# Kernel tuning notes

Measured on AMD Instinct MI355X. Metric: run time of the kernel, lower is better.

Reference implementation:

```python
import jax, jax.numpy as jnp
import numpy as np
from jax import lax

EPS = 1e-5

def _bn_train(x, gamma, beta):
    # BatchNorm2d in training mode: batch stats over (N,H,W), biased variance
    mean = jnp.mean(x, axis=(0, 2, 3), keepdims=True)
    var = jnp.mean((x - mean) ** 2, axis=(0, 2, 3), keepdims=True)
    xhat = (x - mean) * lax.rsqrt(var + EPS)
    return gamma[None, :, None, None] * xhat + beta[None, :, None, None]

def _binact(x):
    # forward: sign(x); backward (STE): identity where |x|<=1, zero elsewhere
    y = jnp.where(jnp.abs(x) > 1.0, lax.stop_gradient(x), x)
    return y + lax.stop_gradient(jnp.sign(y) - y)

def _binconv(x, w, padding):
    # per-output-channel alpha = mean(|w|) over (in,kh,kw); w_bin = sign(w)*alpha with STE
    alpha = jnp.mean(jnp.abs(w), axis=(1, 2, 3), keepdims=True)
    w_bin = lax.stop_gradient(jnp.sign(w) * alpha - w) + w
    return lax.conv_general_dilated(
        x, w_bin, window_strides=(1, 1),
        padding=[(padding, padding), (padding, padding)],
        dimension_numbers=("NCHW", "OIHW", "NCHW"))

def setup_inputs() -> dict:
    key = jax.random.key(0)
    ks = jax.random.split(key, 10)
    B, Cin, Cout, H, W, T = 32, 128, 256, 64, 64, 512
    x = jax.random.normal(ks[0], (B, Cin, H, W), jnp.float32)
    t = jax.random.normal(ks[1], (B, T), jnp.float32)
    # conv weights, kaiming-ish scale
    w1 = jax.random.normal(ks[2], (Cout, Cin, 3, 3), jnp.float32) * (1.0 / np.sqrt(Cin * 9))
    w2 = jax.random.normal(ks[3], (Cout, Cout, 3, 3), jnp.float32) * (1.0 / np.sqrt(Cout * 9))
    wskip = jax.random.normal(ks[4], (Cout, Cin, 1, 1), jnp.float32) * (1.0 / np.sqrt(Cin))
    gamma1 = 1.0 + 0.1 * jax.random.normal(ks[5], (Cin,), jnp.float32)
    beta1 = 0.1 * jax.random.normal(ks[6], (Cin,), jnp.float32)
    gamma2 = 1.0 + 0.1 * jax.random.normal(ks[7], (Cout,), jnp.float32)
    beta2 = 0.1 * jax.random.normal(ks[8], (Cout,), jnp.float32)
    tw = jax.random.normal(ks[9], (Cout, T), jnp.float32) * (1.0 / np.sqrt(T))
    tb = jnp.zeros((Cout,), jnp.float32)
    return {"x": x, "t": t, "w1": w1, "w2": w2, "wskip": wskip,
            "gamma1": gamma1, "beta1": beta1, "gamma2": gamma2, "beta2": beta2,
            "tw": tw, "tb": tb}

def reference(x, t, w1, w2, wskip, gamma1, beta1, gamma2, beta2, tw, tb):
    h = _binconv(_binact(_bn_train(x, gamma1, beta1)), w1, padding=1)
    temb = t @ tw.T + tb                      # [B, Cout]
    h = h + temb[:, :, None, None]
    h = _binconv(_binact(_bn_train(h, gamma2, beta2)), w2, padding=1)
    return h + _binconv(x, wskip, padding=0)
```

## Files before the change

### kernel.cpp

```cpp
#include <hip/hip_runtime.h>
#include <stdint.h>

typedef unsigned short u16;
typedef uint8_t u8;
typedef __attribute__((ext_vector_type(8))) short short8;
typedef __attribute__((ext_vector_type(4))) float f32x4;
typedef __attribute__((ext_vector_type(4))) int i32x4;

#define EPSF 1e-5f
#define LGKM0 asm volatile("s_waitcnt lgkmcnt(0)" ::: "memory")
#define VM0   asm volatile("s_waitcnt vmcnt(0)" ::: "memory")
#define VM4   asm volatile("s_waitcnt vmcnt(4)" ::: "memory")
#define BAR   __builtin_amdgcn_s_barrier()
#define GLL(src, dst) __builtin_amdgcn_global_load_lds(                     \
    (const __attribute__((address_space(1))) void*)(src),                   \
    (__attribute__((address_space(3))) void*)(dst), 16, 0, 0)

__device__ __forceinline__ u16 f2bf(float f) {
  uint32_t u = __float_as_uint(f);
  u += 0x7FFFu + ((u >> 16) & 1u);
  return (u16)(u >> 16);
}
__device__ __forceinline__ u8 sgn8(float y) {
  return y > 0.f ? (u8)1 : (y < 0.f ? (u8)0xFF : (u8)0);
}

__global__ void bn1_stage1(const float* __restrict__ x, float* __restrict__ p1) {
  int c = blockIdx.x >> 2, s = blockIdx.x & 3;
  int tid = threadIdx.x;
  float sum = 0.f, sq = 0.f;
  for (int n = s * 8; n < s * 8 + 8; ++n) {
    const f32x4* bp = (const f32x4*)(x + (((size_t)(n * 128 + c)) << 12));
    #pragma unroll 4
    for (int i = tid; i < 1024; i += 256) {
      f32x4 v = bp[i];
      sum += v[0] + v[1] + v[2] + v[3];
      sq  += v[0]*v[0] + v[1]*v[1] + v[2]*v[2] + v[3]*v[3];
    }
  }
  __shared__ float rs[256], rq[256];
  rs[tid] = sum; rq[tid] = sq; __syncthreads();
  for (int st = 128; st > 0; st >>= 1) {
    if (tid < st) { rs[tid] += rs[tid + st]; rq[tid] += rq[tid + st]; }
    __syncthreads();
  }
  if (tid == 0) { p1[blockIdx.x] = rs[0]; p1[512 + blockIdx.x] = rq[0]; }
}

__global__ void bn1_stage2(const float* __restrict__ p1, const float* __restrict__ g,
                           const float* __restrict__ b, float* __restrict__ sc,
                           float* __restrict__ off) {
  int c = threadIdx.x;
  float s = 0.f, q = 0.f;
  for (int k = 0; k < 4; ++k) { s += p1[c * 4 + k]; q += p1[512 + c * 4 + k]; }
  float mean = s * (1.f / 131072.f);
  float var  = q * (1.f / 131072.f) - mean * mean;
  float is = rsqrtf(var + EPSF);
  float scv = g[c] * is;
  sc[c] = scv;
  off[c] = b[c] - mean * scv;
}

__global__ void bn2_stage2b(const float* __restrict__ pS, const float* __restrict__ pQ,
                            const float* __restrict__ g, const float* __restrict__ bb,
                            float* __restrict__ sc, float* __restrict__ off) {
  int o = blockIdx.x, t = threadIdx.x;
  __shared__ float rs[256], rq[256];
  float s = 0.f, q = 0.f;
  #pragma unroll
  for (int k = 0; k < 8; ++k) {
    size_t j = t + k * 256;
    s += pS[j * 256 + o];
    q += pQ[j * 256 + o];
  }
  rs[t] = s; rq[t] = q; __syncthreads();
  for (int st = 128; st > 0; st >>= 1) {
    if (t < st) { rs[t] += rs[t + st]; rq[t] += rq[t + st]; }
    __syncthreads();
  }
  if (t == 0) {
    float mean = rs[0] * (1.f / 131072.f);
    float var  = rq[0] * (1.f / 131072.f) - mean * mean;
    float is = rsqrtf(var + EPSF);
    float scv = g[o] * is;
    sc[o] = scv;
    off[o] = bb[o] - mean * scv;
  }
}

__device__ __forceinline__ float blk_reduce(float v, float* red) {
  int t = threadIdx.x;
  red[t] = v; __syncthreads();
  for (int st = 128; st > 0; st >>= 1) {
    if (t < st) red[t] += red[t + st];
    __syncthreads();
  }
  float r = red[0]; __syncthreads();
  return r;
}

__global__ void prep_weights(const float* __restrict__ w1, const float* __restrict__ w2,
                             const float* __restrict__ wsk, u8* __restrict__ w1s,
                             u8* __restrict__ w2s, u16* __restrict__ wskB,
                             float* __restrict__ alpha1, float* __restrict__ alpha2) {
  int o = blockIdx.x, t = threadIdx.x;
  int rg = o >> 6, ol = o & 63;
  __shared__ float red[256];
  float s = 0.f;
  for (int j = t; j < 1152; j += 256) s += fabsf(w1[(size_t)o * 1152 + j]);
  float a1 = blk_reduce(s, red) * (1.f / 1152.f);
  if (t == 0) alpha1[o] = a1;
  for (int j = t; j < 1152; j += 256) {
    int st = j >> 6, k = j & 63;
    int cc = st / 9, tap = st % 9;
    int ch = cc * 64 + k;
    int g = (ol << 2) + ((k >> 4) ^ ((ol >> 1) & 3));
    w1s[(size_t)st * 16384 + rg * 4096 + g * 16 + (k & 15)] =
        sgn8(w1[(size_t)o * 1152 + ch * 9 + tap]);
  }
  s = 0.f;
  for (int j = t; j < 2304; j += 256) s += fabsf(w2[(size_t)o * 2304 + j]);
  float a2 = blk_reduce(s, red) * (1.f / 2304.f);
  if (t == 0) alpha2[o] = a2;
  for (int j = t; j < 2304; j += 256) {
    int st = j >> 6, k = j & 63;
    int c4 = st / 9, tap = st % 9;
    int ch = c4 * 64 + k;
    int g = (ol << 2) + ((k >> 4) ^ ((ol >> 1) & 3));
    w2s[(size_t)st * 16384 + rg * 4096 + g * 16 + (k & 15)] =
        sgn8(w2[(size_t)o * 2304 + ch * 9 + tap]);
  }
  s = 0.f;
  for (int j = t; j < 128; j += 256) s += fabsf(wsk[o * 128 + j]);
  float ask = blk_reduce(s, red) * (1.f / 128.f);
  float ratio = ask / a2;
  for (int j = t; j < 128; j += 256) {
    int e = j >> 6, k = j & 63;
    float w = wsk[o * 128 + j];
    float v = w > 0.f ? ratio : (w < 0.f ? -ratio : 0.f);
    wskB[(size_t)e * 16384 + o * 64 + k] = f2bf(v);
  }
}

__global__ void temb_k(const float* __restrict__ t, const float* __restrict__ tw,
                       const float* __restrict__ tb, float* __restrict__ temb) {
  int bb = blockIdx.x, o = threadIdx.x;
  __shared__ float tl[512];
  tl[o] = t[bb * 512 + o];
  tl[o + 256] = t[bb * 512 + 256 + o];
  __syncthreads();
  float acc = tb[o];
  #pragma unroll 8
  for (int k = 0; k < 512; ++k) acc += tl[k] * tw[(size_t)o * 512 + k];
  temb[bb * 256 + o] = acc;
}

__global__ void border_zero(u8* __restrict__ Abuf) {
  u8* plane = Abuf + (size_t)blockIdx.x * 278784;
  int tid = threadIdx.x;
  i32x4 z = {};
  for (int idx = tid; idx < 260; idx += 256) {
    int row, px;
    if (idx < 66) { row = 0; px = idx; }
    else if (idx < 132) { row = 65; px = idx - 66; }
    else { int e = idx - 132; row = 1 + (e >> 1); px = (e & 1) * 65; }
    u8* p = plane + (size_t)(row * 66 + px) * 64;
    #pragma unroll
    for (int i = 0; i < 4; ++i) *(i32x4*)(p + i * 16) = z;
  }
}

__global__ void binact1(const float* __restrict__ x, const float* __restrict__ sc,
                        const float* __restrict__ off, u8* __restrict__ a1p,
                        u16* __restrict__ xb) {
  int b = blockIdx.x >> 6, y = blockIdx.x & 63, tid = threadIdx.x;
  __shared__ u8  ls[64 * 144];
  __shared__ u16 lx[64 * 136];
  int c = tid >> 1, x0 = (tid & 1) * 32;
  const float* src = x + (((size_t)(b * 128 + c)) << 12) + y * 64 + x0;
  float s0 = sc[c], o0 = off[c];
  #pragma unroll
  for (int i = 0; i < 32; i += 4) {
    f32x4 v = *(const f32x4*)(src + i);
    #pragma unroll
    for (int j = 0; j < 4; ++j) {
      int xc = x0 + i + j;
      float yv = s0 * v[j] + o0;
      ls[xc * 144 + c] = sgn8(yv);
      lx[xc * 136 + c] = f2bf(v[j]);
    }
  }
  __syncthreads();
  int xx = tid >> 2, cg = (tid & 3) * 32;
  int cc = cg >> 6, ch0 = cg & 63;
  u8*  pdst = a1p + ((size_t)(b * 2 + cc) * 4356 + (y + 1) * 66 + xx + 1) * 64 + ch0;
  u16* xdst = xb + ((size_t)blockIdx.x * 64 + xx) * 128 + cg;
  *(i32x4*)(pdst)      = *(const i32x4*)&ls[xx * 144 + cg];
  *(i32x4*)(pdst + 16) = *(const i32x4*)&ls[xx * 144 + cg + 16];
  #pragma unroll
  for (int i = 0; i < 32; i += 8)
    *(i32x4*)(xdst + i) = *(const i32x4*)&lx[xx * 136 + cg + i];
}

__global__ void binact2(const float* __restrict__ h, const float* __restrict__ sc,
                        const float* __restrict__ off, u8* __restrict__ a2p) {
  int b = blockIdx.x >> 6, y = blockIdx.x & 63, tid = threadIdx.x;
  __shared__ float s_sc[256], s_off[256];
  s_sc[tid] = sc[tid]; s_off[tid] = off[tid];
  __syncthreads();
  const f32x4* src = (const f32x4*)(h + (size_t)blockIdx.x * 16384);
  #pragma unroll 4
  for (int i = tid; i < 4096; i += 256) {
    f32x4 v = src[i];
    int px = i >> 6, c0 = (i & 63) * 4;
    int c4 = c0 >> 6, chm = c0 & 63;
    uint32_t p = (uint32_t)sgn8(s_sc[c0 + 0] * v[0] + s_off[c0 + 0]) |
                 ((uint32_t)sgn8(s_sc[c0 + 1] * v[1] + s_off[c0 + 1]) << 8) |
                 ((uint32_t)sgn8(s_sc[c0 + 2] * v[2] + s_off[c0 + 2]) << 16) |
                 ((uint32_t)sgn8(s_sc[c0 + 3] * v[3] + s_off[c0 + 3]) << 24);
    u8* dst = a2p + ((size_t)(b * 4 + c4) * 4356 + (y + 1) * 66 + px + 1) * 64 + chm;
    *(uint32_t*)dst = p;
  }
}

template <int NCHUNK, bool SKIP, bool ADD_TEMB, bool STATS, bool DIRECT>
__global__ __launch_bounds__(256, 2) void convk(
    const u8* __restrict__ Apl, const u16* __restrict__ xb,
    const u8* __restrict__ wS, const u16* __restrict__ wskB,
    const float* __restrict__ alpha, const float* __restrict__ temb,
    float* __restrict__ outp, float* __restrict__ pS, float* __restrict__ pQ) {
  constexpr int NS = NCHUNK * 9;
  __shared__ u8 smem[45440];
  u8* lA = smem;
  u8* lB = smem + 12672;
  const int tid = threadIdx.x;
  const int lane = tid & 63, wn = tid >> 6;
  const int kq = lane >> 4, li = lane & 15;

  const int bid = blockIdx.x;
  const int tile = (bid & 7) * 256 + (bid >> 3);
  const int m0 = tile * 64;
  const int b = tile >> 6, y = tile & 63;

  auto issueB = [&](int s) {
    const u8* src = wS + (size_t)s * 16384 + wn * 4096 + lane * 16;
    u8* dst = lB + (s & 1) * 16384 + wn * 4096;
    #pragma unroll
    for (int i = 0; i < 4; ++i) GLL(src + i * 1024, dst + i * 1024);
  };

  auto winLoad = [&](int c) {
    const u8* gp = Apl + (size_t)(b * NCHUNK + c) * 278784 + (size_t)y * 4224;
    #pragma unroll
    for (int k = 0; k < 3; ++k) {
      int g = tid + k * 256;
      int row = g / 264, rem = g - row * 264;
      int px = rem >> 2, sl = rem & 3;
      const u8* src = gp + (size_t)(row * 66 + px) * 64 + ((sl ^ ((px >> 1) & 3)) << 4);
      u8* dst = lA + (size_t)((tid & ~63) + k * 256) * 16;
      GLL(src, dst);
    }
    if (tid < 24) {
      int rem = 240 + tid;
      int px = rem >> 2, sl = rem & 3;
      const u8* src = gp + (size_t)(2 * 66 + px) * 64 + ((sl ^ ((px >> 1) & 3)) << 4);
      GLL(src, lA + (size_t)768 * 16);
    }
  };

  const u8* pA[3];
  #pragma unroll
  for (int dx = 0; dx < 3; ++dx)
    pA[dx] = lA + (li + dx) * 64 + ((kq ^ (((li + dx) >> 1) & 3)) << 4);
  const u8* pB = lB + wn * 4096 + li * 64 + ((kq ^ ((li >> 1) & 3)) << 4);

  i32x4 acc[4][4] = {};

  auto step = [&](int s, i32x4 (&bcur)[4], i32x4 (&bnxt)[4]) {
    if (NCHUNK > 1 && s > 0 && (s % 9) == 0) {
      LGKM0; BAR;
      winLoad(s / 9);
      VM0; BAR;
    }
    LGKM0;
    if (s + 2 < NS) { issueB(s + 2); VM4; }
    else { VM0; }
    const int tap = s % 9, dy = tap / 3, dx = tap % 3;
    i32x4 av[4];
    #pragma unroll
    for (int f = 0; f < 4; ++f)
      av[f] = *(const i32x4*)(pA[dx] + dy * 4224 + f * 1024);
    if (s + 1 < NS) {
      #pragma unroll
      for (int f = 0; f < 4; ++f)
        bnxt[f] = *(const i32x4*)(pB + ((s + 1) & 1) * 16384 + f * 1024);
    }
    __builtin_amdgcn_s_setprio(1);
    #pragma unroll
    for (int mf = 0; mf < 4; ++mf)
      #pragma unroll
      for (int nf = 0; nf < 4; ++nf)
        acc[mf][nf] = __builtin_amdgcn_mfma_i32_16x16x64_i8(
            av[mf], bcur[nf], acc[mf][nf], 0, 0, 0);
    __builtin_amdgcn_s_setprio(0);
  };

  winLoad(0);
  issueB(0);
  issueB(1);
  VM4;
  BAR;
  i32x4 bvA[4], bvB[4];
  #pragma unroll
  for (int f = 0; f < 4; ++f) bvA[f] = *(const i32x4*)(pB + f * 1024);

  #pragma unroll
  for (int s = 0; s < NS; ++s) {
    if ((s & 1) == 0) step(s, bvA, bvB);
    else              step(s, bvB, bvA);
  }

  f32x4 facc[4][4];
  if constexpr (SKIP) {
    #pragma unroll
    for (int mf = 0; mf < 4; ++mf)
      #pragma unroll
      for (int nf = 0; nf < 4; ++nf)
        #pragma unroll
        for (int r = 0; r < 4; ++r)
          facc[mf][nf][r] = (float)acc[mf][nf][r];
    const u8* pAs[2];
    const u8* pBs[2];
    #pragma unroll
    for (int ks = 0; ks < 2; ++ks) {
      pAs[ks] = lA + li * 128 + ((((ks << 2) + kq) ^ (li & 7)) << 4);
      pBs[ks] = lB + (wn * 64 + li) * 128 + ((((ks << 2) + kq) ^ (li & 7)) << 4);
    }
    LGKM0; BAR;
    #pragma unroll
    for (int e = 0; e < 2; ++e) {
      #pragma unroll
      for (int k = 0; k < 2; ++k) {
        int g = tid + k * 256;
        int m = g >> 3, sl = g & 7;
        const u8* src = (const u8*)xb + (size_t)(m0 + m) * 256 + e * 128 +
                        ((sl ^ (m & 7)) << 4);
        u8* dst = lA + (size_t)((tid & ~63) + k * 256) * 16;
        GLL(src, dst);
      }
      i32x4 rS[8];
      const i32x4* gs = (const i32x4*)((const u8*)wskB + (size_t)e * 32768) + tid;
      #pragma unroll
      for (int k = 0; k < 8; ++k) rS[k] = gs[k * 256];
      VM0;
      #pragma unroll
      for (int k = 0; k < 8; ++k) {
        int g = tid + k * 256;
        int o = g >> 3, sl = g & 7;
        *(i32x4*)(lB + o * 128 + ((sl ^ (o & 7)) << 4)) = rS[k];
      }
      LGKM0; BAR;
      #pragma unroll
      for (int ks = 0; ks < 2; ++ks) {
        short8 av[4], bv[4];
        #pragma unroll
        for (int f = 0; f < 4; ++f) av[f] = *(const short8*)(pAs[ks] + f * 2048);
        #pragma unroll
        for (int f = 0; f < 4; ++f) bv[f] = *(const short8*)(pBs[ks] + f * 2048);
        __builtin_amdgcn_s_setprio(1);
        #pragma unroll
        for (int mf = 0; mf < 4; ++mf)
          #pragma unroll
          for (int nf = 0; nf < 4; ++nf)
            facc[mf][nf] = __builtin_amdgcn_mfma_f32_16x16x32_bf16(
                av[mf], bv[nf], facc[mf][nf], 0, 0, 0);
        __builtin_amdgcn_s_setprio(0);
      }
      if (e == 0) { LGKM0; BAR; }
    }
  }

  const int cb = wn * 64 + li;

  if constexpr (STATS) {
    float als[4], tas[4];
    #pragma unroll
    for (int nf = 0; nf < 4; ++nf) {
      int o = cb + nf * 16;
      als[nf] = alpha[o];
      tas[nf] = ADD_TEMB ? temb[b * 256 + o] : 0.f;
    }
    float ps[4] = {0.f, 0.f, 0.f, 0.f}, pq[4] = {0.f, 0.f, 0.f, 0.f};
    #pragma unroll
    for (int nf = 0; nf < 4; ++nf)
      #pragma unroll
      for (int mf = 0; mf < 4; ++mf)
        #pragma unroll
        for (int r = 0; r < 4; ++r) {
          float v = (float)acc[mf][nf][r] * als[nf] + tas[nf];
          ps[nf] += v; pq[nf] += v * v;
        }
    #pragma unroll
    for (int nf = 0; nf < 4; ++nf) {
      ps[nf] += __shfl_xor(ps[nf], 16); ps[nf] += __shfl_xor(ps[nf], 32);
      pq[nf] += __shfl_xor(pq[nf], 16); pq[nf] += __shfl_xor(pq[nf], 32);
    }
    if (lane < 16) {
      #pragma unroll
      for (int nf = 0; nf < 4; ++nf) {
        pS[(size_t)bid * 256 + wn * 64 + nf * 16 + lane] = ps[nf];
        pQ[(size_t)bid * 256 + wn * 64 + nf * 16 + lane] = pq[nf];
      }
    }
    __syncthreads();
    float* ld = (float*)smem;
    const int c3 = li & 3;
    #pragma unroll
    for (int half = 0; half < 2; ++half) {
      #pragma unroll
      for (int mf2 = 0; mf2 < 2; ++mf2) {
        const int mf = half * 2 + mf2;
        #pragma unroll
        for (int nf = 0; nf < 4; ++nf) {
          int colg0 = (cb >> 2) + nf * 4;
          #pragma unroll
          for (int r = 0; r < 4; ++r) {
            int rloc = mf2 * 16 + 4 * kq + r;
            float v = (float)acc[mf][nf][r] * als[nf] + tas[nf];
            ld[rloc * 256 + ((colg0 ^ kq) << 2) + c3] = v;
          }
        }
      }
      __syncthreads();
      #pragma unroll
      for (int it = 0; it < 8; ++it) {
        int flat = tid + it * 256;
        int row = flat >> 6, c4 = flat & 63;
        int c4p = c4 ^ ((row >> 2) & 3);
        f32x4 v = *(const f32x4*)&ld[row * 256 + c4p * 4];
        *(f32x4*)(outp + (size_t)(m0 + half * 32 + row) * 256 + c4 * 4) = v;
      }
      __syncthreads();
    }
  } else if constexpr (DIRECT) {
    float* tb2 = (float*)smem;
    float* obase = outp + (((size_t)(b * 256)) << 12) + (m0 & 4095);
    __syncthreads();
    #pragma unroll
    for (int c4 = 0; c4 < 4; ++c4) {
      if (wn == c4) {
        #pragma unroll
        for (int nf = 0; nf < 4; ++nf) {
          float al = alpha[c4 * 64 + nf * 16 + li];
          #pragma unroll
          for (int mf = 0; mf < 4; ++mf) {
            int cs = (li + nf * 16) ^ ((mf >> 1) & 3);
            #pragma unroll
            for (int r = 0; r < 4; ++r)
              tb2[(mf * 16 + 4 * kq + r) * 65 + cs] = facc[mf][nf][r] * al;
          }
        }
      }
      __syncthreads();
      #pragma unroll
      for (int it = 0; it < 4; ++it) {
        int flat = tid + it * 256;
        int ch = flat >> 4, mg = flat & 15;
        int chs = ch ^ ((mg >> 3) & 3);
        f32x4 v;
        #pragma unroll
        for (int e = 0; e < 4; ++e) v[e] = tb2[(mg * 4 + e) * 65 + chs];
        *(f32x4*)(obase + (((size_t)(c4 * 64 + ch)) << 12) + mg * 4) = v;
      }
      __syncthreads();
    }
  }
}

extern "C" void kernel_launch(void* const* d_in, const int* in_sizes, int n_in,
                              void* d_out, int out_size, void* d_ws, size_t ws_size,
                              hipStream_t stream) {
  const float* x      = (const float*)d_in[0];
  const float* t      = (const float*)d_in[1];
  const float* w1     = (const float*)d_in[2];
  const float* w2     = (const float*)d_in[3];
  const float* wskip  = (const float*)d_in[4];
  const float* gamma1 = (const float*)d_in[5];
  const float* beta1  = (const float*)d_in[6];
  const float* gamma2 = (const float*)d_in[7];
  const float* beta2  = (const float*)d_in[8];
  const float* tw     = (const float*)d_in[9];
  const float* tb     = (const float*)d_in[10];
  float* out = (float*)d_out;

  uint8_t* base = (uint8_t*)d_ws;
  size_t off = 0;
  auto alloc = [&](size_t bytes) {
    void* p = base + off;
    off += (bytes + 255) & ~(size_t)255;
    return p;
  };
  u8* Abuf     = (u8*)alloc((size_t)192 * 278784);
  u8* a1p      = Abuf;
  u8* a2p      = Abuf + (size_t)64 * 278784;
  u16* xb      = (u16*)alloc((size_t)131072 * 128 * 2);
  float* h     = (float*)alloc((size_t)131072 * 256 * 4);
  u8* w1s      = (u8*)alloc((size_t)18 * 16384);
  u8* w2s      = (u8*)alloc((size_t)36 * 16384);
  u16* wskB    = (u16*)alloc((size_t)2 * 16384 * 2);
  float* temb  = (float*)alloc(32 * 256 * 4);
  float* alpha1 = (float*)alloc(256 * 4);
  float* alpha2 = (float*)alloc(256 * 4);
  float* p1    = (float*)alloc(1024 * 4);
  float* pS    = (float*)alloc((size_t)2048 * 256 * 4);
  float* pQ    = (float*)alloc((size_t)2048 * 256 * 4);
  float* sc1   = (float*)alloc(128 * 4);
  float* off1  = (float*)alloc(128 * 4);
  float* sc2   = (float*)alloc(256 * 4);
  float* off2  = (float*)alloc(256 * 4);

  border_zero<<<192, 256, 0, stream>>>(Abuf);

  bn1_stage1<<<512, 256, 0, stream>>>(x, p1);
  bn1_stage2<<<1, 128, 0, stream>>>(p1, gamma1, beta1, sc1, off1);
  prep_weights<<<256, 256, 0, stream>>>(w1, w2, wskip, w1s, w2s, wskB, alpha1, alpha2);
  temb_k<<<32, 256, 0, stream>>>(t, tw, tb, temb);
  binact1<<<2048, 256, 0, stream>>>(x, sc1, off1, a1p, xb);

  convk<2, false, true, true, false><<<2048, 256, 0, stream>>>(
      a1p, xb, w1s, (const u16*)nullptr, alpha1, temb, h, pS, pQ);

  bn2_stage2b<<<256, 256, 0, stream>>>(pS, pQ, gamma2, beta2, sc2, off2);
  binact2<<<2048, 256, 0, stream>>>(h, sc2, off2, a2p);

  convk<4, true, false, false, true><<<2048, 256, 0, stream>>>(
      a2p, xb, w2s, wskB, alpha2, (const float*)nullptr, out,
      (float*)nullptr, (float*)nullptr);

  (void)in_sizes; (void)n_in; (void)out_size; (void)ws_size;
}
```

Measured before the change: 294.6 us.

## Load conv weights directly into registers instead of staging through LDS

Weights are pre-packed into a per-lane register layout so each wave loads its MFMA B operands straight from global memory (L2-resident) into VGPRs, double-buffered two steps ahead. The LDS weight staging buffer is removed, shrinking shared memory from about 45KB to about 17KB, and the skip-conv bf16 weights are loaded the same way. The STATS epilogue is reworked into four 16-row passes to fit the smaller LDS. In exchange it uses more registers, relies on cache hits for repeated weight reads across blocks, and the wait logic becomes coarser (VM0 is used during window reloads).

```diff
diff --git a/kernel.cpp b/kernel.cpp
--- a/kernel.cpp
+++ b/kernel.cpp
@@ -10,7 +10,6 @@
 #define EPSF 1e-5f
 #define LGKM0 asm volatile("s_waitcnt lgkmcnt(0)" ::: "memory")
 #define VM0   asm volatile("s_waitcnt vmcnt(0)" ::: "memory")
-#define VM4   asm volatile("s_waitcnt vmcnt(4)" ::: "memory")
 #define BAR   __builtin_amdgcn_s_barrier()
 #define GLL(src, dst) __builtin_amdgcn_global_load_lds(                     \
     (const __attribute__((address_space(1))) void*)(src),                   \
@@ -100,11 +99,11 @@
 }
 
 __global__ void prep_weights(const float* __restrict__ w1, const float* __restrict__ w2,
-                             const float* __restrict__ wsk, u8* __restrict__ w1s,
-                             u8* __restrict__ w2s, u16* __restrict__ wskB,
+                             const float* __restrict__ wsk, u8* __restrict__ w1r,
+                             u8* __restrict__ w2r, u16* __restrict__ wskr,
                              float* __restrict__ alpha1, float* __restrict__ alpha2) {
   int o = blockIdx.x, t = threadIdx.x;
-  int rg = o >> 6, ol = o & 63;
+  int rg = o >> 6, nf = (o >> 4) & 3, li = o & 15;
   __shared__ float red[256];
   float s = 0.f;
   for (int j = t; j < 1152; j += 256) s += fabsf(w1[(size_t)o * 1152 + j]);
@@ -114,9 +113,9 @@
     int st = j >> 6, k = j & 63;
     int cc = st / 9, tap = st % 9;
     int ch = cc * 64 + k;
-    int g = (ol << 2) + ((k >> 4) ^ ((ol >> 1) & 3));
-    w1s[(size_t)st * 16384 + rg * 4096 + g * 16 + (k & 15)] =
-        sgn8(w1[(size_t)o * 1152 + ch * 9 + tap]);
+    size_t idx = ((size_t)((st * 4 + rg) * 64 + (k >> 4) * 16 + li)) * 64 +
+                 nf * 16 + (k & 15);
+    w1r[idx] = sgn8(w1[(size_t)o * 1152 + ch * 9 + tap]);
   }
   s = 0.f;
   for (int j = t; j < 2304; j += 256) s += fabsf(w2[(size_t)o * 2304 + j]);
@@ -126,19 +125,21 @@
     int st = j >> 6, k = j & 63;
     int c4 = st / 9, tap = st % 9;
     int ch = c4 * 64 + k;
-    int g = (ol << 2) + ((k >> 4) ^ ((ol >> 1) & 3));
-    w2s[(size_t)st * 16384 + rg * 4096 + g * 16 + (k & 15)] =
-        sgn8(w2[(size_t)o * 2304 + ch * 9 + tap]);
+    size_t idx = ((size_t)((st * 4 + rg) * 64 + (k >> 4) * 16 + li)) * 64 +
+                 nf * 16 + (k & 15);
+    w2r[idx] = sgn8(w2[(size_t)o * 2304 + ch * 9 + tap]);
   }
   s = 0.f;
   for (int j = t; j < 128; j += 256) s += fabsf(wsk[o * 128 + j]);
   float ask = blk_reduce(s, red) * (1.f / 128.f);
   float ratio = ask / a2;
   for (int j = t; j < 128; j += 256) {
-    int e = j >> 6, k = j & 63;
+    int e = j >> 6, c = j & 63;
+    int ks = c >> 5, kq = (c >> 3) & 3, jj = c & 7;
     float w = wsk[o * 128 + j];
     float v = w > 0.f ? ratio : (w < 0.f ? -ratio : 0.f);
-    wskB[(size_t)e * 16384 + o * 64 + k] = f2bf(v);
+    wskr[((size_t)((e * 4 + rg) * 64 + kq * 16 + li)) * 64 + (ks * 4 + nf) * 8 + jj] =
+        f2bf(v);
   }
 }
 
@@ -226,13 +227,12 @@
 template <int NCHUNK, bool SKIP, bool ADD_TEMB, bool STATS, bool DIRECT>
 __global__ __launch_bounds__(256, 2) void convk(
     const u8* __restrict__ Apl, const u16* __restrict__ xb,
-    const u8* __restrict__ wS, const u16* __restrict__ wskB,
+    const u8* __restrict__ wB, const u16* __restrict__ wskr,
     const float* __restrict__ alpha, const float* __restrict__ temb,
     float* __restrict__ outp, float* __restrict__ pS, float* __restrict__ pQ) {
   constexpr int NS = NCHUNK * 9;
-  __shared__ u8 smem[45440];
+  __shared__ u8 smem[16896];
   u8* lA = smem;
-  u8* lB = smem + 12672;
   const int tid = threadIdx.x;
   const int lane = tid & 63, wn = tid >> 6;
   const int kq = lane >> 4, li = lane & 15;
@@ -242,11 +242,11 @@
   const int m0 = tile * 64;
   const int b = tile >> 6, y = tile & 63;
 
-  auto issueB = [&](int s) {
-    const u8* src = wS + (size_t)s * 16384 + wn * 4096 + lane * 16;
-    u8* dst = lB + (s & 1) * 16384 + wn * 4096;
-    #pragma unroll
-    for (int i = 0; i < 4; ++i) GLL(src + i * 1024, dst + i * 1024);
+  const i32x4* wlane = (const i32x4*)(wB + ((size_t)wn * 64 + lane) * 64);
+  auto loadB = [&](int s, i32x4 (&dst)[4]) {
+    const i32x4* src = wlane + (size_t)s * 1024;
+    #pragma unroll
+    for (int i = 0; i < 4; ++i) dst[i] = src[i];
   };
 
   auto winLoad = [&](int c) {
@@ -272,29 +272,15 @@
   #pragma unroll
   for (int dx = 0; dx < 3; ++dx)
     pA[dx] = lA + (li + dx) * 64 + ((kq ^ (((li + dx) >> 1) & 3)) << 4);
-  const u8* pB = lB + wn * 4096 + li * 64 + ((kq ^ ((li >> 1) & 3)) << 4);
 
   i32x4 acc[4][4] = {};
 
-  auto step = [&](int s, i32x4 (&bcur)[4], i32x4 (&bnxt)[4]) {
-    if (NCHUNK > 1 && s > 0 && (s % 9) == 0) {
-      LGKM0; BAR;
-      winLoad(s / 9);
-      VM0; BAR;
-    }
-    LGKM0;
-    if (s + 2 < NS) { issueB(s + 2); VM4; }
-    else { VM0; }
+  auto compute = [&](int s, i32x4 (&bcur)[4]) {
     const int tap = s % 9, dy = tap / 3, dx = tap % 3;
     i32x4 av[4];
     #pragma unroll
     for (int f = 0; f < 4; ++f)
       av[f] = *(const i32x4*)(pA[dx] + dy * 4224 + f * 1024);
-    if (s + 1 < NS) {
-      #pragma unroll
-      for (int f = 0; f < 4; ++f)
-        bnxt[f] = *(const i32x4*)(pB + ((s + 1) & 1) * 16384 + f * 1024);
-    }
     __builtin_amdgcn_s_setprio(1);
     #pragma unroll
     for (int mf = 0; mf < 4; ++mf)
@@ -306,18 +292,26 @@
   };
 
   winLoad(0);
-  issueB(0);
-  issueB(1);
-  VM4;
+  i32x4 bA[4], bB[4];
+  loadB(0, bA);
+  loadB(1, bB);
+  VM0;
   BAR;
-  i32x4 bvA[4], bvB[4];
-  #pragma unroll
-  for (int f = 0; f < 4; ++f) bvA[f] = *(const i32x4*)(pB + f * 1024);
 
   #pragma unroll
   for (int s = 0; s < NS; ++s) {
-    if ((s & 1) == 0) step(s, bvA, bvB);
-    else              step(s, bvB, bvA);
+    if (NCHUNK > 1 && s > 0 && (s % 9) == 0) {
+      LGKM0; BAR;
+      winLoad(s / 9);
+      VM0; BAR;
+    }
+    if ((s & 1) == 0) {
+      compute(s, bA);
+      if (s + 2 < NS) loadB(s + 2, bA);
+    } else {
+      compute(s, bB);
+      if (s + 2 < NS) loadB(s + 2, bB);
+    }
   }
 
   f32x4 facc[4][4];
@@ -330,12 +324,9 @@
         for (int r = 0; r < 4; ++r)
           facc[mf][nf][r] = (float)acc[mf][nf][r];
     const u8* pAs[2];
-    const u8* pBs[2];
-    #pragma unroll
-    for (int ks = 0; ks < 2; ++ks) {
+    #pragma unroll
+    for (int ks = 0; ks < 2; ++ks)
       pAs[ks] = lA + li * 128 + ((((ks << 2) + kq) ^ (li & 7)) << 4);
-      pBs[ks] = lB + (wn * 64 + li) * 128 + ((((ks << 2) + kq) ^ (li & 7)) << 4);
-    }
     LGKM0; BAR;
     #pragma unroll
     for (int e = 0; e < 2; ++e) {
@@ -348,32 +339,23 @@
         u8* dst = lA + (size_t)((tid & ~63) + k * 256) * 16;
         GLL(src, dst);
       }
-      i32x4 rS[8];
-      const i32x4* gs = (const i32x4*)((const u8*)wskB + (size_t)e * 32768) + tid;
-      #pragma unroll
-      for (int k = 0; k < 8; ++k) rS[k] = gs[k * 256];
-      VM0;
-      #pragma unroll
-      for (int k = 0; k < 8; ++k) {
-        int g = tid + k * 256;
-        int o = g >> 3, sl = g & 7;
-        *(i32x4*)(lB + o * 128 + ((sl ^ (o & 7)) << 4)) = rS[k];
-      }
-      LGKM0; BAR;
+      const u16* bbase = wskr + ((size_t)(e * 4 + wn) * 64 + lane) * 64;
+      short8 sb[8];
+      #pragma unroll
+      for (int i = 0; i < 8; ++i) sb[i] = *(const short8*)(bbase + i * 8);
+      VM0; BAR;
       #pragma unroll
       for (int ks = 0; ks < 2; ++ks) {
-        short8 av[4], bv[4];
+        short8 av[4];
         #pragma unroll
         for (int f = 0; f < 4; ++f) av[f] = *(const short8*)(pAs[ks] + f * 2048);
-        #pragma unroll
-        for (int f = 0; f < 4; ++f) bv[f] = *(const short8*)(pBs[ks] + f * 2048);
         __builtin_amdgcn_s_setprio(1);
         #pragma unroll
         for (int mf = 0; mf < 4; ++mf)
           #pragma unroll
           for (int nf = 0; nf < 4; ++nf)
             facc[mf][nf] = __builtin_amdgcn_mfma_f32_16x16x32_bf16(
-                av[mf], bv[nf], facc[mf][nf], 0, 0, 0);
+                av[mf], sb[ks * 4 + nf], facc[mf][nf], 0, 0, 0);
         __builtin_amdgcn_s_setprio(0);
       }
       if (e == 0) { LGKM0; BAR; }
@@ -416,29 +398,25 @@
     float* ld = (float*)smem;
     const int c3 = li & 3;
     #pragma unroll
-    for (int half = 0; half < 2; ++half) {
-      #pragma unroll
-      for (int mf2 = 0; mf2 < 2; ++mf2) {
-        const int mf = half * 2 + mf2;
-        #pragma unroll
-        for (int nf = 0; nf < 4; ++nf) {
-          int colg0 = (cb >> 2) + nf * 4;
-          #pragma unroll
-          for (int r = 0; r < 4; ++r) {
-            int rloc = mf2 * 16 + 4 * kq + r;
-            float v = (float)acc[mf][nf][r] * als[nf] + tas[nf];
-            ld[rloc * 256 + ((colg0 ^ kq) << 2) + c3] = v;
-          }
+    for (int p = 0; p < 4; ++p) {
+      #pragma unroll
+      for (int nf = 0; nf < 4; ++nf) {
+        int colg0 = (cb >> 2) + nf * 4;
+        #pragma unroll
+        for (int r = 0; r < 4; ++r) {
+          int rloc = 4 * kq + r;
+          float v = (float)acc[p][nf][r] * als[nf] + tas[nf];
+          ld[rloc * 256 + ((colg0 ^ kq) << 2) + c3] = v;
         }
       }
       __syncthreads();
       #pragma unroll
-      for (int it = 0; it < 8; ++it) {
+      for (int it = 0; it < 4; ++it) {
         int flat = tid + it * 256;
         int row = flat >> 6, c4 = flat & 63;
         int c4p = c4 ^ ((row >> 2) & 3);
         f32x4 v = *(const f32x4*)&ld[row * 256 + c4p * 4];
-        *(f32x4*)(outp + (size_t)(m0 + half * 32 + row) * 256 + c4 * 4) = v;
+        *(f32x4*)(outp + (size_t)(m0 + p * 16 + row) * 256 + c4 * 4) = v;
       }
       __syncthreads();
     }
@@ -505,9 +483,9 @@
   u8* a2p      = Abuf + (size_t)64 * 278784;
   u16* xb      = (u16*)alloc((size_t)131072 * 128 * 2);
   float* h     = (float*)alloc((size_t)131072 * 256 * 4);
-  u8* w1s      = (u8*)alloc((size_t)18 * 16384);
-  u8* w2s      = (u8*)alloc((size_t)36 * 16384);
-  u16* wskB    = (u16*)alloc((size_t)2 * 16384 * 2);
+  u8* w1r      = (u8*)alloc((size_t)18 * 16384);
+  u8* w2r      = (u8*)alloc((size_t)36 * 16384);
+  u16* wskr    = (u16*)alloc((size_t)2 * 16384 * 2);
   float* temb  = (float*)alloc(32 * 256 * 4);
   float* alpha1 = (float*)alloc(256 * 4);
   float* alpha2 = (float*)alloc(256 * 4);
@@ -523,18 +501,18 @@
 
   bn1_stage1<<<512, 256, 0, stream>>>(x, p1);
   bn1_stage2<<<1, 128, 0, stream>>>(p1, gamma1, beta1, sc1, off1);
-  prep_weights<<<256, 256, 0, stream>>>(w1, w2, wskip, w1s, w2s, wskB, alpha1, alpha2);
+  prep_weights<<<256, 256, 0, stream>>>(w1, w2, wskip, w1r, w2r, wskr, alpha1, alpha2);
   temb_k<<<32, 256, 0, stream>>>(t, tw, tb, temb);
   binact1<<<2048, 256, 0, stream>>>(x, sc1, off1, a1p, xb);
 
   convk<2, false, true, true, false><<<2048, 256, 0, stream>>>(
-      a1p, xb, w1s, (const u16*)nullptr, alpha1, temb, h, pS, pQ);
+      a1p, xb, w1r, (const u16*)nullptr, alpha1, temb, h, pS, pQ);
 
   bn2_stage2b<<<256, 256, 0, stream>>>(pS, pQ, gamma2, beta2, sc2, off2);
   binact2<<<2048, 256, 0, stream>>>(h, sc2, off2, a2p);
 
   convk<4, true, false, false, true><<<2048, 256, 0, stream>>>(
-      a2p, xb, w2s, wskB, alpha2, (const float*)nullptr, out,
+      a2p, xb, w2r, wskr, alpha2, (const float*)nullptr, out,
       (float*)nullptr, (float*)nullptr);
 
   (void)in_sizes; (void)n_in; (void)out_size; (void)ws_size;
```

Result: slower. 305.2 us (+3.6%).
